# Kernel tuning notes

Measured on AMD Instinct MI355X. Metric: run time of the kernel, lower is better.

Reference implementation:

```python
import jax, jax.numpy as jnp
import numpy as np

N_HEAD = 16

def _phi(x):
    # silu(x) + 1 feature map
    return jax.nn.silu(x) + 1.0

def setup_inputs() -> dict:
    key = jax.random.key(0)
    ks = jax.random.split(key, 8)
    B, T, D = 8, 4096, 1024
    s = 0.02
    return {
        "x":  jax.random.normal(ks[0], (B, T, D), jnp.float32),
        "Wq": jax.random.normal(ks[1], (D, D), jnp.float32) * s,
        "bq": jax.random.normal(ks[2], (D,), jnp.float32) * s,
        "Wk": jax.random.normal(ks[3], (D, D), jnp.float32) * s,
        "Wv": jax.random.normal(ks[4], (D, D), jnp.float32) * s,
        "bv": jax.random.normal(ks[5], (D,), jnp.float32) * s,
        "Wo": jax.random.normal(ks[6], (D, D), jnp.float32) * s,
        "bo": jax.random.normal(ks[7], (D,), jnp.float32) * s,
    }

def reference(x, Wq, bq, Wk, Wv, bv, Wo, bo):
    B, T, D = x.shape
    H = N_HEAD
    Dh = D // H
    scale = Dh ** (-0.25)
    # projections (torch F.linear: x @ W.T + b); key has no bias
    q = x @ Wq.T + bq
    k = x @ Wk.T
    v = x @ Wv.T + bv
    # [B, T, H, Dh] -> [B, H, T, Dh]
    q = q.reshape(B, T, H, Dh).transpose(0, 2, 1, 3) * scale
    k = k.reshape(B, T, H, Dh).transpose(0, 2, 1, 3) * scale
    v = v.reshape(B, T, H, Dh).transpose(0, 2, 1, 3)
    phi_q = _phi(q)
    phi_k = _phi(k)
    # kv: [B, H, Dh, Dh] = sum_t phi_k[t]^T v[t]
    kv = jnp.einsum('bhtd,bhte->bhde', phi_k, v)
    out = jnp.einsum('bhtd,bhde->bhte', phi_q, kv)  # [B, H, T, Dh]
    wv = out.transpose(0, 2, 1, 3).reshape(B, T, D)
    return wv @ Wo.T + bo
```

## Files before the change

kernel.cpp:

```cpp
#include <hip/hip_runtime.h>
#include <math.h>

typedef short bf16x8 __attribute__((ext_vector_type(8)));
typedef float f32x4  __attribute__((ext_vector_type(4)));

__device__ __forceinline__ float phi_act(float t) {
    return t / (1.0f + __expf(-t)) + 1.0f;
}

__device__ __forceinline__ unsigned short f2bf(float f) {
    union { float f; unsigned int u; } un; un.f = f;
    unsigned int r = un.u + 0x7fffu + ((un.u >> 16) & 1u);
    return (unsigned short)(r >> 16);
}

__device__ __forceinline__ void gload_lds16(const void* g, void* l) {
    __builtin_amdgcn_global_load_lds(
        (const __attribute__((address_space(1))) void*)g,
        (__attribute__((address_space(3))) void*)l, 16, 0, 0);
}


__device__ __forceinline__ void stage2(const char* g, int voff0, int voff1,
                                       char* l, int wb16) {
    gload_lds16(g + voff0, l + wb16);
    gload_lds16(g + voff1, l + 8192 + wb16);
}

#define LOAD_AF(buf, ah) do {                                                   \
    const char* _s = (const char*)&As[buf][ah][0];                              \
    _Pragma("unroll")                                                           \
    for (int _mi = 0; _mi < 4; _mi++) {                                         \
        const int _row = qm * 64 + _mi * 16 + ml;                               \
        const int _sw = (_row & 7) << 4;                                        \
        _Pragma("unroll")                                                       \
        for (int _ks = 0; _ks < 2; _ks++)                                       \
            af[_mi][_ks] = *(const bf16x8*)(_s +                                \
                (((_row * 128) + _ks * 64 + kq * 16) ^ _sw));                   \
    }                                                                           \
} while (0)

#define LOAD_BF_TO(dst, buf, bh) do {                                           \
    const char* _s = (const char*)&Bs[buf][bh][0];                              \
    _Pragma("unroll")                                                           \
    for (int _nj = 0; _nj < 2; _nj++) {                                         \
        const int _col = qn * 32 + _nj * 16 + ml;                               \
        const int _sw = (_col & 7) << 4;                                        \
        _Pragma("unroll")                                                       \
        for (int _ks = 0; _ks < 2; _ks++)                                       \
            dst[_nj][_ks] = *(const bf16x8*)(_s +                               \
                (((_col * 128) + _ks * 64 + kq * 16) ^ _sw));                   \
    }                                                                           \
} while (0)

#define MFMA_Q(Q, B) do {                                                       \
    __builtin_amdgcn_s_setprio(1);                                              \
    _Pragma("unroll")                                                           \
    for (int _mi = 0; _mi < 4; _mi++)                                           \
        _Pragma("unroll")                                                       \
        for (int _nj = 0; _nj < 2; _nj++)                                       \
            _Pragma("unroll")                                                   \
            for (int _ks = 0; _ks < 2; _ks++)                                   \
                acc[Q][_mi][_nj] = __builtin_amdgcn_mfma_f32_16x16x32_bf16(     \
                    af[_mi][_ks], B[_nj][_ks], acc[Q][_mi][_nj], 0, 0, 0);      \
    __builtin_amdgcn_s_setprio(0);                                              \
} while (0)

template<int KIND>
__device__ __forceinline__ void gemm256_body(
    const unsigned short* __restrict__ A, const unsigned short* __restrict__ W,
    const float* __restrict__ bq, const float* __restrict__ bv,
    unsigned short* __restrict__ oq, unsigned short* __restrict__ okk,
    unsigned short* __restrict__ ov, float* __restrict__ outF,
    const float* __restrict__ bo, float scale, int NBN)
{
    __shared__ __align__(128) unsigned short As[2][2][128 * 64];
    __shared__ __align__(128) unsigned short Bs[2][2][128 * 64];

    const int tid  = threadIdx.x;
    const int lane = tid & 63;
    const int w    = tid >> 6;
    const int qm   = w >> 2;
    const int qn   = w & 3;
    const int ml   = lane & 15;
    const int kq   = lane >> 4;

    const int nwg  = (int)gridDim.x;
    const int bid  = (int)blockIdx.x;
    const int sbid = (bid & 7) * (nwg >> 3) + (bid >> 3);
    const int bn   = sbid % NBN;
    const int bm   = sbid / NBN;

    const char* pA = (const char*)(A + (size_t)bm * 256 * 1024);
    const unsigned short* Wbase =
        (KIND == 1) ? (W + (size_t)(bm >> 4) * 1024 * 1024) : W;
    const char* pB = (const char*)(Wbase + (size_t)bn * 256 * 1024);

    int voff[2];
    #pragma unroll
    for (int u = 0; u < 2; u++) {
        const int p  = (u * 512 + tid) * 16;
        const int qq = p ^ (((p >> 7) & 7) << 4);
        voff[u] = (qq >> 7) * 2048 + (qq & 127);
    }
    const int wb16 = (tid & ~63) * 16;

    f32x4 acc[4][4][2];
    f32x4 zero4 = {0.f, 0.f, 0.f, 0.f};
    #pragma unroll
    for (int q = 0; q < 4; q++)
        #pragma unroll
        for (int mi = 0; mi < 4; mi++)
            #pragma unroll
            for (int nj = 0; nj < 2; nj++) acc[q][mi][nj] = zero4;

    bf16x8 af[4][2], bf0[2][2], bf1[2][2];

    stage2(pA,              voff[0], voff[1], (char*)&As[0][0][0], wb16);
    stage2(pB,              voff[0], voff[1], (char*)&Bs[0][0][0], wb16);
    stage2(pB + 256 * 1024, voff[0], voff[1], (char*)&Bs[0][1][0], wb16);
    stage2(pA + 256 * 1024, voff[0], voff[1], (char*)&As[0][1][0], wb16);

    for (int t = 0; t < 16; ++t) {
        const int buf = t & 1;
        const char* A0n = pA + (size_t)(t + 1) * 128;
        const char* A1n = A0n + 256 * 1024;
        const char* B0n = pB + (size_t)(t + 1) * 128;
        const char* B1n = B0n + 256 * 1024;
        const bool st = (t + 1 < 16);

        asm volatile("s_waitcnt vmcnt(4)" ::: "memory");
        __builtin_amdgcn_s_barrier();
        asm volatile("" ::: "memory");
        LOAD_AF(buf, 0);
        LOAD_BF_TO(bf0, buf, 0);
        if (st) {
            stage2(A0n, voff[0], voff[1], (char*)&As[buf ^ 1][0][0], wb16);
            stage2(B0n, voff[0], voff[1], (char*)&Bs[buf ^ 1][0][0], wb16);
        }
        asm volatile("s_waitcnt lgkmcnt(0)" ::: "memory");
        MFMA_Q(0, bf0);

        if (st) { asm volatile("s_waitcnt vmcnt(6)" ::: "memory"); }
        else    { asm volatile("s_waitcnt vmcnt(2)" ::: "memory"); }
        __builtin_amdgcn_s_barrier();
        asm volatile("" ::: "memory");
        LOAD_BF_TO(bf1, buf, 1);
        if (st) stage2(B1n, voff[0], voff[1], (char*)&Bs[buf ^ 1][1][0], wb16);
        asm volatile("s_waitcnt lgkmcnt(0)" ::: "memory");
        MFMA_Q(1, bf1);

        if (st) { asm volatile("s_waitcnt vmcnt(6)" ::: "memory"); }
        else    { asm volatile("s_waitcnt vmcnt(0)" ::: "memory"); }
        __builtin_amdgcn_s_barrier();
        asm volatile("" ::: "memory");
        LOAD_AF(buf, 1);
        if (st) stage2(A1n, voff[0], voff[1], (char*)&As[buf ^ 1][1][0], wb16);
        asm volatile("s_waitcnt lgkmcnt(0)" ::: "memory");
        MFMA_Q(2, bf1);

        MFMA_Q(3, bf0);
    }

    const int rq = lane >> 4, cl = lane & 15;
    #pragma unroll
    for (int q = 0; q < 4; q++) {
        const int qr = (q >> 1) * 128;
        const int qc = ((q == 1) || (q == 2)) ? 128 : 0;
        #pragma unroll
        for (int nj = 0; nj < 2; nj++) {
            const int colg = bn * 256 + qc + qn * 32 + nj * 16 + cl;
            if constexpr (KIND == 0) {
                const int z    = colg >> 10;
                const int lcol = colg & 1023;
                const float bias = (z == 0) ? bq[lcol] : ((z == 2) ? bv[lcol] : 0.f);
                unsigned short* dst = (z == 0) ? oq : ((z == 1) ? okk : ov);
                #pragma unroll
                for (int mi = 0; mi < 4; mi++) {
                    const int row0 = bm * 256 + qr + qm * 64 + mi * 16 + rq * 4;
                    #pragma unroll
                    for (int r = 0; r < 4; r++) {
                        float vv = acc[q][mi][nj][r] + bias;
                        if (z < 2) vv = phi_act(vv * scale);
                        dst[(size_t)(row0 + r) * 1024 + lcol] = f2bf(vv);
                    }
                }
            } else {
                const float bias = bo[colg];
                #pragma unroll
                for (int mi = 0; mi < 4; mi++) {
                    const int row0 = bm * 256 + qr + qm * 64 + mi * 16 + rq * 4;
                    #pragma unroll
                    for (int r = 0; r < 4; r++)
                        outF[(size_t)(row0 + r) * 1024 + colg] = acc[q][mi][nj][r] + bias;
                }
            }
        }
    }
}

__global__ __launch_bounds__(512, 2) void qkv_gemm256(
    const unsigned short* __restrict__ xb,
    const unsigned short* __restrict__ wcat,
    const float* __restrict__ bq, const float* __restrict__ bv,
    unsigned short* __restrict__ phiq, unsigned short* __restrict__ phik,
    unsigned short* __restrict__ vb, float scale)
{
    gemm256_body<0>(xb, wcat, bq, bv, phiq, phik, vb, nullptr, nullptr, scale, 12);
}

__global__ __launch_bounds__(512, 2) void out_gemm256(
    const unsigned short* __restrict__ A, const unsigned short* __restrict__ W,
    const float* __restrict__ bo, float* __restrict__ out)
{
    gemm256_body<1>(A, W, nullptr, nullptr, nullptr, nullptr, nullptr, out, bo, 1.0f, 4);
}

__global__ __launch_bounds__(256) void cast_all(
    const float* __restrict__ x,  unsigned short* __restrict__ xb,
    const float* __restrict__ w0, unsigned short* __restrict__ w0b,
    const float* __restrict__ w1, unsigned short* __restrict__ w1b,
    const float* __restrict__ w2, unsigned short* __restrict__ w2b,
    const float* __restrict__ w3, unsigned short* __restrict__ w3b,
    size_t nx, size_t nw)
{
    size_t i = ((size_t)blockIdx.x * 256 + threadIdx.x) * 4;
    const float* s; unsigned short* d; size_t off;
    if (i < nx)               { s = x;  d = xb;  off = i; }
    else if (i < nx + nw)     { s = w0; d = w0b; off = i - nx; }
    else if (i < nx + 2 * nw) { s = w1; d = w1b; off = i - nx - nw; }
    else if (i < nx + 3 * nw) { s = w2; d = w2b; off = i - nx - 2 * nw; }
    else                      { s = w3; d = w3b; off = i - nx - 3 * nw; }
    float4 v = *(const float4*)(s + off);
    ushort4 o;
    o.x = f2bf(v.x); o.y = f2bf(v.y); o.z = f2bf(v.z); o.w = f2bf(v.w);
    *(ushort4*)(d + off) = o;
}

__global__ __launch_bounds__(256) void kv_part(
    const unsigned short* __restrict__ phiK, const unsigned short* __restrict__ V,
    float* __restrict__ partial, int Ttot, int D)
{
    const int tc = blockIdx.x, bh = blockIdx.y;
    const int b = bh >> 4, h = bh & 15;
    const int tbase = tc * 512;

    __shared__ unsigned short pkT[64][72];
    __shared__ unsigned short vvT[64][72];

    const int tid  = threadIdx.x;
    const int lane = tid & 63;
    const int w    = tid >> 6;
    const int dq = w >> 1, eq = w & 1;
    const int kq = lane >> 4, ml = lane & 15;

    const int tq  = tid >> 3;
    const int oct = tid & 7;
    const int d8  = oct * 8;
    const int tw0 = (tq * 2) ^ (oct << 3);

    f32x4 zero4 = {0.f, 0.f, 0.f, 0.f};
    f32x4 acc[2][2];
    acc[0][0] = zero4; acc[0][1] = zero4; acc[1][0] = zero4; acc[1][1] = zero4;

    const size_t base = (size_t)b * Ttot * D + h * 64;

#define PACKW(arr, lo, hi, i0)                                                   \
    *(unsigned int*)&arr[d8 + i0    ][tw0] = ((lo) & 0xffffu) | ((hi) << 16);    \
    *(unsigned int*)&arr[d8 + i0 + 1][tw0] = ((lo) >> 16) | ((hi) & 0xffff0000u);

    for (int c8 = 0; c8 < 8; c8++) {
        const int t0 = tbase + c8 * 64;
        __syncthreads();
        {
            const size_t g0 = base + (size_t)(t0 + tq * 2) * D + d8;
            uint4 k0 = *(const uint4*)(phiK + g0);
            uint4 k1 = *(const uint4*)(phiK + g0 + D);
            uint4 v0 = *(const uint4*)(V + g0);
            uint4 v1 = *(const uint4*)(V + g0 + D);
            PACKW(pkT, k0.x, k1.x, 0) PACKW(pkT, k0.y, k1.y, 2)
            PACKW(pkT, k0.z, k1.z, 4) PACKW(pkT, k0.w, k1.w, 6)
            PACKW(vvT, v0.x, v1.x, 0) PACKW(vvT, v0.y, v1.y, 2)
            PACKW(vvT, v0.z, v1.z, 4) PACKW(vvT, v0.w, v1.w, 6)
        }
        __syncthreads();

        #pragma unroll
        for (int ks = 0; ks < 2; ks++) {
            bf16x8 af[2], bfv[2];
            #pragma unroll
            for (int ai = 0; ai < 2; ai++) {
                const int row = dq * 32 + ai * 16 + ml;
                const int col = ((ks * 4 + kq) ^ ((row >> 3) & 7)) << 3;
                af[ai] = *(const bf16x8*)&pkT[row][col];
            }
            #pragma unroll
            for (int bi = 0; bi < 2; bi++) {
                const int row = eq * 32 + bi * 16 + ml;
                const int col = ((ks * 4 + kq) ^ ((row >> 3) & 7)) << 3;
                bfv[bi] = *(const bf16x8*)&vvT[row][col];
            }
            #pragma unroll
            for (int ai = 0; ai < 2; ai++)
                #pragma unroll
                for (int bi = 0; bi < 2; bi++)
                    acc[ai][bi] = __builtin_amdgcn_mfma_f32_16x16x32_bf16(
                        af[ai], bfv[bi], acc[ai][bi], 0, 0, 0);
        }
    }
#undef PACKW

    float* outp = partial + ((size_t)bh * 8 + tc) * 4096;
    const int rq = lane >> 4, cl = lane & 15;
    #pragma unroll
    for (int ai = 0; ai < 2; ai++)
        #pragma unroll
        for (int bi = 0; bi < 2; bi++) {
            const int e = eq * 32 + bi * 16 + cl;
            #pragma unroll
            for (int r = 0; r < 4; r++) {
                const int d = dq * 32 + ai * 16 + rq * 4 + r;
                outp[d * 64 + e] = acc[ai][bi][r];
            }
        }
}

__global__ __launch_bounds__(256) void kv_weff(
    const float* __restrict__ partial, const unsigned short* __restrict__ wob,
    unsigned short* __restrict__ weff)
{
    const int bh = blockIdx.x;
    const int b = bh >> 4, h = bh & 15;

    __shared__ unsigned short kvs[64][72];
    __shared__ __align__(128) unsigned short Awo[128 * 64];

    const int tid  = threadIdx.x;
    const int lane = tid & 63;
    const int w    = tid >> 6;
    const int ml = lane & 15, kq = lane >> 4;

    {
        float a[16];
        #pragma unroll
        for (int c = 0; c < 16; c++) a[c] = 0.f;
        #pragma unroll
        for (int p = 0; p < 8; p++) {
            const float* src = partial + ((size_t)bh * 8 + p) * 4096;
            #pragma unroll
            for (int c = 0; c < 16; c++) a[c] += src[c * 256 + tid];
        }
        #pragma unroll
        for (int c = 0; c < 16; c++) {
            const int idx = c * 256 + tid;
            kvs[idx >> 6][idx & 63] = f2bf(a[c]);
        }
    }
    __syncthreads();

    bf16x8 bfv[4][2];
    #pragma unroll
    for (int nj = 0; nj < 4; nj++)
        #pragma unroll
        for (int ks = 0; ks < 2; ks++)
            bfv[nj][ks] = *(const bf16x8*)&kvs[nj * 16 + ml][ks * 32 + kq * 8];

    int voff[4];
    #pragma unroll
    for (int u = 0; u < 4; u++) {
        const int p  = (u * 256 + tid) * 16;
        const int qq = p ^ (((p >> 7) & 7) << 4);
        voff[u] = (qq >> 7) * 2048 + (qq & 127);
    }
    const int wb = tid & ~63;
    const char* gsrc = (const char*)wob + (size_t)h * 128;
    unsigned short* dstb = weff + (size_t)b * 1024 * 1024 + h * 64;
    const int rq = lane >> 4, cl = lane & 15;

    for (int oc = 0; oc < 8; ++oc) {
        __syncthreads();
        #pragma unroll
        for (int u = 0; u < 4; u++)
            gload_lds16(gsrc + (size_t)oc * 128 * 2048 + voff[u],
                        (char*)Awo + (size_t)(u * 256 + wb) * 16);
        asm volatile("s_waitcnt vmcnt(0)" ::: "memory");
        __syncthreads();

        bf16x8 af[2][2];
        #pragma unroll
        for (int mi = 0; mi < 2; mi++) {
            const int r128 = w * 32 + mi * 16 + ml;
            const int sw = (r128 & 7) << 4;
            #pragma unroll
            for (int ks = 0; ks < 2; ks++)
                af[mi][ks] = *(const bf16x8*)((const char*)Awo +
                    (((r128 * 128) + ks * 64 + kq * 16) ^ sw));
        }

        f32x4 acc[2][4];
        f32x4 zero4 = {0.f, 0.f, 0.f, 0.f};
        #pragma unroll
        for (int mi = 0; mi < 2; mi++)
            #pragma unroll
            for (int nj = 0; nj < 4; nj++) acc[mi][nj] = zero4;

        #pragma unroll
        for (int ks = 0; ks < 2; ks++)
            #pragma unroll
            for (int mi = 0; mi < 2; mi++)
                #pragma unroll
                for (int nj = 0; nj < 4; nj++)
                    acc[mi][nj] = __builtin_amdgcn_mfma_f32_16x16x32_bf16(
                        af[mi][ks], bfv[nj][ks], acc[mi][nj], 0, 0, 0);

        #pragma unroll
        for (int mi = 0; mi < 2; mi++)
            #pragma unroll
            for (int nj = 0; nj < 4; nj++)
                #pragma unroll
                for (int r = 0; r < 4; r++) {
                    const int o = oc * 128 + w * 32 + mi * 16 + rq * 4 + r;
                    dstb[(size_t)o * 1024 + nj * 16 + cl] = f2bf(acc[mi][nj][r]);
                }
    }
}

extern "C" void kernel_launch(void* const* d_in, const int* in_sizes, int n_in,
                              void* d_out, int out_size, void* d_ws, size_t ws_size,
                              hipStream_t stream) {
    const float* x  = (const float*)d_in[0];
    const float* Wq = (const float*)d_in[1];
    const float* bq = (const float*)d_in[2];
    const float* Wk = (const float*)d_in[3];
    const float* Wv = (const float*)d_in[4];
    const float* bv = (const float*)d_in[5];
    const float* Wo = (const float*)d_in[6];
    const float* bo = (const float*)d_in[7];
    float* out = (float*)d_out;

    const int B = 8, T = 4096, D = 1024;
    const int M = B * T;
    const float scale = 0.35355339059327379f;
    const size_t MD = (size_t)M * D;
    const size_t WN = (size_t)D * D;

    unsigned short* xb    = (unsigned short*)d_ws;
    unsigned short* wqb   = xb + MD;
    unsigned short* wkb   = wqb + WN;
    unsigned short* wvb   = wkb + WN;
    unsigned short* wob   = wvb + WN;
    unsigned short* phiq  = wob + WN;
    unsigned short* phik  = phiq + MD;
    unsigned short* vb    = phik + MD;
    unsigned short* weff  = vb + MD;
    float*          part  = (float*)(weff + (size_t)8 * 1024 * 1024);
    (void)ws_size; (void)in_sizes; (void)n_in; (void)out_size;

    dim3 blk(256);

    {
        size_t total4 = (MD + 4 * WN) / 4;
        cast_all<<<dim3((unsigned)(total4 / 256)), blk, 0, stream>>>(
            x, xb, Wq, wqb, Wk, wkb, Wv, wvb, Wo, wob, MD, WN);
    }

    qkv_gemm256<<<dim3(1536), dim3(512), 0, stream>>>(
        xb, wqb, bq, bv, phiq, phik, vb, scale);

    kv_part<<<dim3(8, 128), blk, 0, stream>>>(phik, vb, part, T, D);
    kv_weff<<<dim3(128), blk, 0, stream>>>(part, wob, weff);

    out_gemm256<<<dim3(512), dim3(512), 0, stream>>>(phiq, weff, bo, out);
}
```

Measured before the change: 584.7 us.

## Fuse kv partial and W_eff kernels with last-block atomic reduction

Merges the kv partial-sum kernel and the W_eff kernel into one launch. Each block writes its partial, bumps a per-head atomic counter, and the last block to finish does the reduction and the Wo multiply. Wo is now read as fp32 straight from global memory and converted in registers, so the separate Wo cast and LDS staging go away. This removes one launch and a global round-trip, but adds a memset and leaves the W_eff tail on only 128 blocks that read fp32 Wo without LDS reuse.

Result: slower. 867.7 us (+48.4%).

```diff
diff --git a/kernel.cpp b/kernel.cpp
--- a/kernel.cpp
+++ b/kernel.cpp
@@ -221,7 +221,6 @@
     const float* __restrict__ w0, unsigned short* __restrict__ w0b,
     const float* __restrict__ w1, unsigned short* __restrict__ w1b,
     const float* __restrict__ w2, unsigned short* __restrict__ w2b,
-    const float* __restrict__ w3, unsigned short* __restrict__ w3b,
     size_t nx, size_t nw)
 {
     size_t i = ((size_t)blockIdx.x * 256 + threadIdx.x) * 4;
@@ -229,17 +228,18 @@
     if (i < nx)               { s = x;  d = xb;  off = i; }
     else if (i < nx + nw)     { s = w0; d = w0b; off = i - nx; }
     else if (i < nx + 2 * nw) { s = w1; d = w1b; off = i - nx - nw; }
-    else if (i < nx + 3 * nw) { s = w2; d = w2b; off = i - nx - 2 * nw; }
-    else                      { s = w3; d = w3b; off = i - nx - 3 * nw; }
+    else                      { s = w2; d = w2b; off = i - nx - 2 * nw; }
     float4 v = *(const float4*)(s + off);
     ushort4 o;
     o.x = f2bf(v.x); o.y = f2bf(v.y); o.z = f2bf(v.z); o.w = f2bf(v.w);
     *(ushort4*)(d + off) = o;
 }
 
-__global__ __launch_bounds__(256) void kv_part(
+__global__ __launch_bounds__(256) void kv_fused(
     const unsigned short* __restrict__ phiK, const unsigned short* __restrict__ V,
-    float* __restrict__ partial, int Ttot, int D)
+    const float* __restrict__ Wo, float* __restrict__ partial,
+    unsigned int* __restrict__ cnt, unsigned short* __restrict__ weff,
+    int Ttot, int D)
 {
     const int tc = blockIdx.x, bh = blockIdx.y;
     const int b = bh >> 4, h = bh & 15;
@@ -247,6 +247,8 @@
 
     __shared__ unsigned short pkT[64][72];
     __shared__ unsigned short vvT[64][72];
+    __shared__ unsigned short kvs[64][72];
+    __shared__ unsigned int is_last;
 
     const int tid  = threadIdx.x;
     const int lane = tid & 63;
@@ -287,12 +289,12 @@
 
         #pragma unroll
         for (int ks = 0; ks < 2; ks++) {
-            bf16x8 af[2], bfv[2];
+            bf16x8 afr[2], bfv[2];
             #pragma unroll
             for (int ai = 0; ai < 2; ai++) {
                 const int row = dq * 32 + ai * 16 + ml;
                 const int col = ((ks * 4 + kq) ^ ((row >> 3) & 7)) << 3;
-                af[ai] = *(const bf16x8*)&pkT[row][col];
+                afr[ai] = *(const bf16x8*)&pkT[row][col];
             }
             #pragma unroll
             for (int bi = 0; bi < 2; bi++) {
@@ -305,40 +307,35 @@
                 #pragma unroll
                 for (int bi = 0; bi < 2; bi++)
                     acc[ai][bi] = __builtin_amdgcn_mfma_f32_16x16x32_bf16(
-                        af[ai], bfv[bi], acc[ai][bi], 0, 0, 0);
+                        afr[ai], bfv[bi], acc[ai][bi], 0, 0, 0);
         }
     }
 #undef PACKW
 
-    float* outp = partial + ((size_t)bh * 8 + tc) * 4096;
-    const int rq = lane >> 4, cl = lane & 15;
-    #pragma unroll
-    for (int ai = 0; ai < 2; ai++)
-        #pragma unroll
-        for (int bi = 0; bi < 2; bi++) {
-            const int e = eq * 32 + bi * 16 + cl;
-            #pragma unroll
-            for (int r = 0; r < 4; r++) {
-                const int d = dq * 32 + ai * 16 + rq * 4 + r;
-                outp[d * 64 + e] = acc[ai][bi][r];
+    {
+        float* outp = partial + ((size_t)bh * 8 + tc) * 4096;
+        const int rq = lane >> 4, cl = lane & 15;
+        #pragma unroll
+        for (int ai = 0; ai < 2; ai++)
+            #pragma unroll
+            for (int bi = 0; bi < 2; bi++) {
+                const int e = eq * 32 + bi * 16 + cl;
+                #pragma unroll
+                for (int r = 0; r < 4; r++) {
+                    const int d = dq * 32 + ai * 16 + rq * 4 + r;
+                    outp[d * 64 + e] = acc[ai][bi][r];
+                }
             }
-        }
-}
-
-__global__ __launch_bounds__(256) void kv_weff(
-    const float* __restrict__ partial, const unsigned short* __restrict__ wob,
-    unsigned short* __restrict__ weff)
-{
-    const int bh = blockIdx.x;
-    const int b = bh >> 4, h = bh & 15;
-
-    __shared__ unsigned short kvs[64][72];
-    __shared__ __align__(128) unsigned short Awo[128 * 64];
-
-    const int tid  = threadIdx.x;
-    const int lane = tid & 63;
-    const int w    = tid >> 6;
-    const int ml = lane & 15, kq = lane >> 4;
+    }
+
+    __threadfence();
+    if (tid == 0) {
+        unsigned int old = atomicAdd(&cnt[bh], 1u);
+        is_last = (old == 7u) ? 1u : 0u;
+    }
+    __syncthreads();
+    if (!is_last) return;
+    __threadfence();
 
     {
         float a[16];
@@ -358,51 +355,41 @@
     }
     __syncthreads();
 
-    bf16x8 bfv[4][2];
+    bf16x8 bkv[4][2];
     #pragma unroll
     for (int nj = 0; nj < 4; nj++)
         #pragma unroll
         for (int ks = 0; ks < 2; ks++)
-            bfv[nj][ks] = *(const bf16x8*)&kvs[nj * 16 + ml][ks * 32 + kq * 8];
-
-    int voff[4];
-    #pragma unroll
-    for (int u = 0; u < 4; u++) {
-        const int p  = (u * 256 + tid) * 16;
-        const int qq = p ^ (((p >> 7) & 7) << 4);
-        voff[u] = (qq >> 7) * 2048 + (qq & 127);
-    }
-    const int wb = tid & ~63;
-    const char* gsrc = (const char*)wob + (size_t)h * 128;
+            bkv[nj][ks] = *(const bf16x8*)&kvs[nj * 16 + ml][ks * 32 + kq * 8];
+
     unsigned short* dstb = weff + (size_t)b * 1024 * 1024 + h * 64;
+    const float* wsl = Wo + (size_t)h * 64;
     const int rq = lane >> 4, cl = lane & 15;
 
     for (int oc = 0; oc < 8; ++oc) {
-        __syncthreads();
-        #pragma unroll
-        for (int u = 0; u < 4; u++)
-            gload_lds16(gsrc + (size_t)oc * 128 * 2048 + voff[u],
-                        (char*)Awo + (size_t)(u * 256 + wb) * 16);
-        asm volatile("s_waitcnt vmcnt(0)" ::: "memory");
-        __syncthreads();
-
-        bf16x8 af[2][2];
+        bf16x8 awo[2][2];
         #pragma unroll
         for (int mi = 0; mi < 2; mi++) {
-            const int r128 = w * 32 + mi * 16 + ml;
-            const int sw = (r128 & 7) << 4;
-            #pragma unroll
-            for (int ks = 0; ks < 2; ks++)
-                af[mi][ks] = *(const bf16x8*)((const char*)Awo +
-                    (((r128 * 128) + ks * 64 + kq * 16) ^ sw));
-        }
-
-        f32x4 acc[2][4];
-        f32x4 zero4 = {0.f, 0.f, 0.f, 0.f};
+            const int o = oc * 128 + w * 32 + mi * 16 + ml;
+            #pragma unroll
+            for (int ks = 0; ks < 2; ks++) {
+                const float* p = wsl + (size_t)o * 1024 + ks * 32 + kq * 8;
+                float4 f0 = *(const float4*)p;
+                float4 f1 = *(const float4*)(p + 4);
+                bf16x8 a;
+                a[0] = (short)f2bf(f0.x); a[1] = (short)f2bf(f0.y);
+                a[2] = (short)f2bf(f0.z); a[3] = (short)f2bf(f0.w);
+                a[4] = (short)f2bf(f1.x); a[5] = (short)f2bf(f1.y);
+                a[6] = (short)f2bf(f1.z); a[7] = (short)f2bf(f1.w);
+                awo[mi][ks] = a;
+            }
+        }
+
+        f32x4 acc2[2][4];
         #pragma unroll
         for (int mi = 0; mi < 2; mi++)
             #pragma unroll
-            for (int nj = 0; nj < 4; nj++) acc[mi][nj] = zero4;
+            for (int nj = 0; nj < 4; nj++) acc2[mi][nj] = zero4;
 
         #pragma unroll
         for (int ks = 0; ks < 2; ks++)
@@ -410,8 +397,8 @@
             for (int mi = 0; mi < 2; mi++)
                 #pragma unroll
                 for (int nj = 0; nj < 4; nj++)
-                    acc[mi][nj] = __builtin_amdgcn_mfma_f32_16x16x32_bf16(
-                        af[mi][ks], bfv[nj][ks], acc[mi][nj], 0, 0, 0);
+                    acc2[mi][nj] = __builtin_amdgcn_mfma_f32_16x16x32_bf16(
+                        awo[mi][ks], bkv[nj][ks], acc2[mi][nj], 0, 0, 0);
 
         #pragma unroll
         for (int mi = 0; mi < 2; mi++)
@@ -420,7 +407,7 @@
                 #pragma unroll
                 for (int r = 0; r < 4; r++) {
                     const int o = oc * 128 + w * 32 + mi * 16 + rq * 4 + r;
-                    dstb[(size_t)o * 1024 + nj * 16 + cl] = f2bf(acc[mi][nj][r]);
+                    dstb[(size_t)o * 1024 + nj * 16 + cl] = f2bf(acc2[mi][nj][r]);
                 }
     }
 }
@@ -448,27 +435,29 @@
     unsigned short* wqb   = xb + MD;
     unsigned short* wkb   = wqb + WN;
     unsigned short* wvb   = wkb + WN;
-    unsigned short* wob   = wvb + WN;
-    unsigned short* phiq  = wob + WN;
+    unsigned short* phiq  = wvb + WN;
     unsigned short* phik  = phiq + MD;
     unsigned short* vb    = phik + MD;
     unsigned short* weff  = vb + MD;
     float*          part  = (float*)(weff + (size_t)8 * 1024 * 1024);
+    unsigned int*   cnt   = (unsigned int*)(part + (size_t)1024 * 4096);
     (void)ws_size; (void)in_sizes; (void)n_in; (void)out_size;
 
     dim3 blk(256);
 
+    hipMemsetAsync(cnt, 0, 128 * sizeof(unsigned int), stream);
+
     {
-        size_t total4 = (MD + 4 * WN) / 4;
+        size_t total4 = (MD + 3 * WN) / 4;
         cast_all<<<dim3((unsigned)(total4 / 256)), blk, 0, stream>>>(
-            x, xb, Wq, wqb, Wk, wkb, Wv, wvb, Wo, wob, MD, WN);
+            x, xb, Wq, wqb, Wk, wkb, Wv, wvb, MD, WN);
     }
 
     qkv_gemm256<<<dim3(1536), dim3(512), 0, stream>>>(
         xb, wqb, bq, bv, phiq, phik, vb, scale);
 
-    kv_part<<<dim3(8, 128), blk, 0, stream>>>(phik, vb, part, T, D);
-    kv_weff<<<dim3(128), blk, 0, stream>>>(part, wob, weff);
+    kv_fused<<<dim3(8, 128), blk, 0, stream>>>(
+        phik, vb, Wo, part, cnt, weff, T, D);
 
     out_gemm256<<<dim3(512), dim3(512), 0, stream>>>(phiq, weff, bo, out);
 }
```
